# Performance work log

Measured on AMD Instinct MI355X. Metric: run time of the kernel, lower is better.

Reference implementation:

```python
import jax, jax.numpy as jnp
import numpy as np

DIM = 1024
HEADS = 16
B, N = 4, 1024

def setup_inputs() -> dict:
    key = jax.random.key(0)
    k1, k2, k3 = jax.random.split(key, 3)
    x = jax.random.normal(k1, (B, N, DIM), dtype=jnp.float32)
    # xavier-uniform-ish init scale
    Wqkv = jax.random.normal(k2, (3 * DIM, DIM), dtype=jnp.float32) * (1.0 / np.sqrt(DIM))
    bqkv = jnp.zeros((3 * DIM,), dtype=jnp.float32)
    W1 = jax.random.normal(k3, (DIM, DIM), dtype=jnp.float32) * (1.0 / np.sqrt(DIM))
    b1 = jnp.zeros((DIM,), dtype=jnp.float32)
    return {"x": x, "Wqkv": Wqkv, "bqkv": bqkv, "W1": W1, "b1": b1}

def reference(x, Wqkv, bqkv, W1, b1):
    b, n, dim = x.shape
    h = HEADS
    d = dim // h
    scale = dim ** (-0.5)  # NOTE: module scales by full dim, not head dim
    qkv = x @ Wqkv.T + bqkv  # [b, n, 3*dim]
    qkv = qkv.reshape(b, n, 3, h, d)
    q = jnp.transpose(qkv[:, :, 0], (0, 2, 1, 3))  # [b, h, n, d]
    k = jnp.transpose(qkv[:, :, 1], (0, 2, 1, 3))
    v = jnp.transpose(qkv[:, :, 2], (0, 2, 1, 3))
    dots = jnp.einsum('bhid,bhjd->bhij', q, k) * scale
    attn = jax.nn.softmax(dots, axis=-1)
    out = jnp.einsum('bhij,bhjd->bhid', attn, v)
    out = jnp.transpose(out, (0, 2, 1, 3)).reshape(b, n, dim)
    out = out @ W1.T + b1
    return out
```

## Files before the change

kernel.cpp:

```cpp
#include <hip/hip_runtime.h>
#include <cmath>

typedef __bf16 bf16;
typedef __bf16 bf16x8 __attribute__((ext_vector_type(8)));
typedef __bf16 bf16x4 __attribute__((ext_vector_type(4)));
typedef float f32x4 __attribute__((ext_vector_type(4)));

#define MFMA16(a, b, c) __builtin_amdgcn_mfma_f32_16x16x32_bf16(a, b, c, 0, 0, 0)

__device__ __forceinline__ void load_lds16(const void* g, void* l) {
    __builtin_amdgcn_global_load_lds(
        (const __attribute__((address_space(1))) void*)g,
        (__attribute__((address_space(3))) void*)l, 16, 0, 0);
}

__device__ __forceinline__ bf16x8 load8(const bf16* p) { return *(const bf16x8*)p; }
__device__ __forceinline__ bf16x8 load8(const float* p) {
    float4 f0 = *(const float4*)p;
    float4 f1 = *(const float4*)(p + 4);
    bf16x8 r;
    r[0] = (bf16)f0.x; r[1] = (bf16)f0.y; r[2] = (bf16)f0.z; r[3] = (bf16)f0.w;
    r[4] = (bf16)f1.x; r[5] = (bf16)f1.y; r[6] = (bf16)f1.z; r[7] = (bf16)f1.w;
    return r;
}

__global__ __launch_bounds__(256) void cvt3(
    const float* __restrict__ s0, bf16* __restrict__ d0, int n0,
    const float* __restrict__ s1, bf16* __restrict__ d1, int n1,
    const float* __restrict__ s2, bf16* __restrict__ d2, int n2)
{
    int i = blockIdx.x * 256 + threadIdx.x;
    const float* s; bf16* d; int base;
    if (i < n0)                { s = s0; d = d0; base = i; }
    else if (i < n0 + n1)      { s = s1; d = d1; base = i - n0; }
    else if (i < n0 + n1 + n2) { s = s2; d = d2; base = i - n0 - n1; }
    else return;
    *(bf16x8*)(d + (size_t)base * 8) = load8(s + (size_t)base * 8);
}

template <int EPI, typename TB, int BN>
__global__ __launch_bounds__(256) void gemm_bt(
    const bf16* __restrict__ A, const TB* __restrict__ Bm,
    const float* __restrict__ bias,
    bf16* __restrict__ qo, bf16* __restrict__ ko, bf16* __restrict__ vto,
    float* __restrict__ C, int M, int N, int K)
{
    constexpr int WN = BN / 2;
    constexpr int JN = WN / 16;
    constexpr int SLOTS = (128 + BN) * 8;

    __shared__ bf16 As[128 * 64];
    __shared__ bf16 Bs[BN * 64];

    const int tid = threadIdx.x;
    const int l   = tid & 63;
    const int w   = tid >> 6;
    const int wm  = w & 1, wn = w >> 1;
    const int l15 = l & 15;
    const int g   = l >> 4;
    const int swz = l15 & 7;
    const int m0  = blockIdx.y * 128;
    const int n0  = blockIdx.x * BN;

    f32x4 acc[4][JN] = {};

    for (int k0 = 0; k0 < K; k0 += 64) {
        __syncthreads();
        #pragma unroll
        for (int it = 0; it < SLOTS / 256; ++it) {
            int s = it * 256 + w * 64 + l;
            if (s < 1024) {
                int row = s >> 3, pc = s & 7;
                int lc  = pc ^ (row & 7);
                load_lds16(A + (size_t)(m0 + row) * K + k0 + lc * 8, &As[s * 8]);
            } else {
                int t = s - 1024;
                int row = t >> 3, pc = t & 7;
                int lc  = pc ^ (row & 7);
                if constexpr (sizeof(TB) == 2) {
                    load_lds16(Bm + (size_t)(n0 + row) * K + k0 + lc * 8, &Bs[t * 8]);
                } else {
                    *(bf16x8*)&Bs[t * 8] = load8(Bm + (size_t)(n0 + row) * K + k0 + lc * 8);
                }
            }
        }
        __syncthreads();
        #pragma unroll
        for (int kk = 0; kk < 64; kk += 32) {
            bf16x8 aF[4], bF[JN];
            #pragma unroll
            for (int i = 0; i < 4; ++i)
                aF[i] = *(const bf16x8*)&As[(wm * 64 + i * 16 + l15) * 64
                                            + ((((kk >> 3) + g) ^ swz) * 8)];
            #pragma unroll
            for (int j = 0; j < JN; ++j)
                bF[j] = *(const bf16x8*)&Bs[(wn * WN + j * 16 + l15) * 64
                                            + ((((kk >> 3) + g) ^ swz) * 8)];
            #pragma unroll
            for (int i = 0; i < 4; ++i)
                #pragma unroll
                for (int j = 0; j < JN; ++j)
                    acc[i][j] = MFMA16(aF[i], bF[j], acc[i][j]);
        }
    }

    #pragma unroll
    for (int j = 0; j < JN; ++j) {
        int gcol = n0 + wn * WN + j * 16 + l15;
        float bv = bias[gcol];
        if (EPI == 0) {
            int which = gcol >> 10;
            int h  = (gcol >> 6) & 15;
            int dd = gcol & 63;
            if (which == 2) {
                #pragma unroll
                for (int i = 0; i < 4; ++i) {
                    int grow0 = m0 + wm * 64 + i * 16 + g * 4;
                    int b     = grow0 >> 10;
                    int npos  = grow0 & 1023;
                    size_t bh = (size_t)(b * 16 + h);
                    bf16x4 pv;
                    #pragma unroll
                    for (int r = 0; r < 4; ++r)
                        pv[r] = (bf16)(acc[i][j][r] + bv);
                    *(bf16x4*)&vto[(bh * 64 + dd) * 1024 + npos] = pv;
                }
            } else {
                #pragma unroll
                for (int i = 0; i < 4; ++i) {
                    #pragma unroll
                    for (int r = 0; r < 4; ++r) {
                        int grow = m0 + wm * 64 + i * 16 + g * 4 + r;
                        int b    = grow >> 10;
                        int npos = grow & 1023;
                        float v  = acc[i][j][r] + bv;
                        size_t bh = (size_t)(b * 16 + h);
                        if (which == 0)
                            qo[(bh * 1024 + npos) * 64 + dd] = (bf16)v;
                        else
                            ko[(bh * 1024 + npos) * 64 + dd] = (bf16)v;
                    }
                }
            }
        } else {
            #pragma unroll
            for (int i = 0; i < 4; ++i)
                #pragma unroll
                for (int r = 0; r < 4; ++r) {
                    int grow = m0 + wm * 64 + i * 16 + g * 4 + r;
                    C[(size_t)grow * N + gcol] = acc[i][j][r] + bv;
                }
        }
    }
}

__global__ __launch_bounds__(256) void attn_fused(
    const bf16* __restrict__ qb, const bf16* __restrict__ kb,
    const bf16* __restrict__ vtb, bf16* __restrict__ attn)
{
    __shared__ bf16 Ks[2][64 * 64];
    __shared__ bf16 Vts[2][64 * 64];
    __shared__ bf16 Ps[4][16][40];

    const int tid = threadIdx.x;
    const int l   = tid & 63;
    const int w   = tid >> 6;
    const int l15 = l & 15;
    const int g   = l >> 4;
    const int swz = l15 & 7;
    const int bid = blockIdx.x;
    const int bh  = bid & 63;
    const int qc  = bid >> 6;
    const int m0  = qc * 64;

    const bf16* q_bh  = qb  + (size_t)bh * 65536;
    const bf16* k_bh  = kb  + (size_t)bh * 65536;
    const bf16* vt_bh = vtb + (size_t)bh * 65536;

    bf16x8 qf[2];
    #pragma unroll
    for (int kk = 0; kk < 2; ++kk)
        qf[kk] = *(const bf16x8*)(q_bh + (size_t)(m0 + w * 16 + l15) * 64
                                  + kk * 32 + g * 8);

    f32x4 o[4] = {};
    float lsum = 0.f;

    const float C_EXP = 0.04508422f;

    auto stage = [&](int buf, int j0) {
        #pragma unroll
        for (int it = 0; it < 2; ++it) {
            int s   = it * 256 + w * 64 + l;
            int row = s >> 3, pc = s & 7;
            int lc  = pc ^ (row & 7);
            load_lds16(k_bh + (size_t)(j0 + row) * 64 + lc * 8, &Ks[buf][s * 8]);
            load_lds16(vt_bh + (size_t)row * 1024 + j0 + lc * 8, &Vts[buf][s * 8]);
        }
    };

    stage(0, 0);

    for (int t = 0; t < 16; ++t) {
        const int c = t & 1;
        __syncthreads();
        if (t < 15) stage(c ^ 1, (t + 1) * 64);

        f32x4 s4[4] = {};
        #pragma unroll
        for (int kk = 0; kk < 2; ++kk) {
            bf16x8 kf[4];
            #pragma unroll
            for (int js = 0; js < 4; ++js)
                kf[js] = *(const bf16x8*)&Ks[c][(js * 16 + l15) * 64
                                                + (((kk * 4 + g) ^ swz) * 8)];
            __builtin_amdgcn_s_setprio(1);
            #pragma unroll
            for (int js = 0; js < 4; ++js)
                s4[js] = MFMA16(kf[js], qf[kk], s4[js]);
            __builtin_amdgcn_s_setprio(0);
        }

        #pragma unroll
        for (int h = 0; h < 2; ++h) {
            #pragma unroll
            for (int jsl = 0; jsl < 2; ++jsl) {
                int js = h * 2 + jsl;
                bf16x4 pk;
                float ps = 0.f;
                #pragma unroll
                for (int r = 0; r < 4; ++r) {
                    float p = exp2f(s4[js][r] * C_EXP);
                    ps += p;
                    pk[r] = (bf16)p;
                }
                lsum += ps;
                *(bf16x4*)&Ps[w][l15][jsl * 16 + g * 4] = pk;
            }
            bf16x8 vf[4];
            #pragma unroll
            for (int ns = 0; ns < 4; ++ns)
                vf[ns] = *(const bf16x8*)&Vts[c][(ns * 16 + l15) * 64
                                                 + (((h * 4 + g) ^ swz) * 8)];
            bf16x8 pf = *(const bf16x8*)&Ps[w][l15][g * 8];
            __builtin_amdgcn_s_setprio(1);
            #pragma unroll
            for (int ns = 0; ns < 4; ++ns)
                o[ns] = MFMA16(pf, vf[ns], o[ns]);
            __builtin_amdgcn_s_setprio(0);
        }
    }

    float t = lsum;
    t += __shfl_xor(t, 16);
    t += __shfl_xor(t, 32);

    #pragma unroll
    for (int r = 0; r < 4; ++r) {
        float inv = 1.0f / __shfl(t, g * 4 + r);
        int grow = m0 + w * 16 + g * 4 + r;
        size_t obase = ((size_t)(bh >> 4) * 1024 + grow) * 1024 + (bh & 15) * 64;
        #pragma unroll
        for (int ns = 0; ns < 4; ++ns)
            attn[obase + ns * 16 + l15] = (bf16)(o[ns][r] * inv);
    }
}

extern "C" void kernel_launch(void* const* d_in, const int* in_sizes, int n_in,
                              void* d_out, int out_size, void* d_ws, size_t ws_size,
                              hipStream_t stream)
{
    const float* x    = (const float*)d_in[0];
    const float* Wqkv = (const float*)d_in[1];
    const float* bqkv = (const float*)d_in[2];
    const float* W1   = (const float*)d_in[3];
    const float* b1   = (const float*)d_in[4];
    float* out = (float*)d_out;

    const size_t SEG = (size_t)4 * 16 * 1024 * 64;
    bf16* xbf  = (bf16*)d_ws;
    bf16* qb   = xbf + SEG;
    bf16* kb   = qb + SEG;
    bf16* vtb  = kb + SEG;
    bf16* attnb = xbf;
    bf16* wqkvbf = vtb + SEG;
    bf16* w1bf   = wqkvbf + 3145728;

    const bool cw = ws_size >= (size_t)(5 * SEG) * sizeof(bf16);

    const int nx = 524288;
    const int nw = cw ? 393216 : 0;
    const int n1 = cw ? 131072 : 0;
    const int tot = nx + nw + n1;
    cvt3<<<dim3((tot + 255) / 256), 256, 0, stream>>>(
        x, xbf, nx, Wqkv, wqkvbf, nw, W1, w1bf, n1);

    if (cw)
        gemm_bt<0, bf16, 128><<<dim3(24, 32), 256, 0, stream>>>(
            xbf, wqkvbf, bqkv, qb, kb, vtb, nullptr, 4096, 3072, 1024);
    else
        gemm_bt<0, float, 128><<<dim3(24, 32), 256, 0, stream>>>(
            xbf, Wqkv, bqkv, qb, kb, vtb, nullptr, 4096, 3072, 1024);

    attn_fused<<<dim3(1024), 256, 0, stream>>>(qb, kb, vtb, attnb);

    if (cw)
        gemm_bt<1, bf16, 64><<<dim3(16, 32), 256, 0, stream>>>(
            attnb, w1bf, b1, nullptr, nullptr, nullptr, out, 4096, 1024, 1024);
    else
        gemm_bt<1, float, 64><<<dim3(16, 32), 256, 0, stream>>>(
            attnb, W1, b1, nullptr, nullptr, nullptr, out, 4096, 1024, 1024);
}
```

Before: 166.1 us.

## Split attention KV tile across two warp halves with LDS reduction

The attention kernel now launches 512 threads per block. Each pair of waves shares the same 16 query rows but handles half of the key columns in each 64-key tile, so per-wave work per tile drops by half. The partial outputs and denominators are then summed through LDS at the end. The P staging buffer also gets an XOR swizzle in place of padding to avoid bank conflicts. This raises the number of active waves to hide latency, at the cost of a final cross-wave reduction and extra barriers.

```diff
diff --git a/kernel.cpp b/kernel.cpp
--- a/kernel.cpp
+++ b/kernel.cpp
@@ -154,17 +154,19 @@
     }
 }
 
-__global__ __launch_bounds__(256) void attn_fused(
+__global__ __launch_bounds__(512, 8) void attn_fused(
     const bf16* __restrict__ qb, const bf16* __restrict__ kb,
     const bf16* __restrict__ vtb, bf16* __restrict__ attn)
 {
     __shared__ bf16 Ks[2][64 * 64];
     __shared__ bf16 Vts[2][64 * 64];
-    __shared__ bf16 Ps[4][16][40];
+    __shared__ bf16 Ps[8][16][32];
 
     const int tid = threadIdx.x;
     const int l   = tid & 63;
     const int w   = tid >> 6;
+    const int wq  = w & 3;
+    const int wh  = w >> 2;
     const int l15 = l & 15;
     const int g   = l >> 4;
     const int swz = l15 & 7;
@@ -180,7 +182,7 @@
     bf16x8 qf[2];
     #pragma unroll
     for (int kk = 0; kk < 2; ++kk)
-        qf[kk] = *(const bf16x8*)(q_bh + (size_t)(m0 + w * 16 + l15) * 64
+        qf[kk] = *(const bf16x8*)(q_bh + (size_t)(m0 + wq * 16 + l15) * 64
                                   + kk * 32 + g * 8);
 
     f32x4 o[4] = {};
@@ -189,14 +191,11 @@
     const float C_EXP = 0.04508422f;
 
     auto stage = [&](int buf, int j0) {
-        #pragma unroll
-        for (int it = 0; it < 2; ++it) {
-            int s   = it * 256 + w * 64 + l;
-            int row = s >> 3, pc = s & 7;
-            int lc  = pc ^ (row & 7);
-            load_lds16(k_bh + (size_t)(j0 + row) * 64 + lc * 8, &Ks[buf][s * 8]);
-            load_lds16(vt_bh + (size_t)row * 1024 + j0 + lc * 8, &Vts[buf][s * 8]);
-        }
+        int s   = tid;
+        int row = s >> 3, pc = s & 7;
+        int lc  = pc ^ (row & 7);
+        load_lds16(k_bh + (size_t)(j0 + row) * 64 + lc * 8, &Ks[buf][s * 8]);
+        load_lds16(vt_bh + (size_t)row * 1024 + j0 + lc * 8, &Vts[buf][s * 8]);
     };
 
     stage(0, 0);
@@ -206,63 +205,78 @@
         __syncthreads();
         if (t < 15) stage(c ^ 1, (t + 1) * 64);
 
-        f32x4 s4[4] = {};
+        f32x4 s4[2] = {};
         #pragma unroll
         for (int kk = 0; kk < 2; ++kk) {
-            bf16x8 kf[4];
-            #pragma unroll
-            for (int js = 0; js < 4; ++js)
-                kf[js] = *(const bf16x8*)&Ks[c][(js * 16 + l15) * 64
-                                                + (((kk * 4 + g) ^ swz) * 8)];
+            bf16x8 kf[2];
+            #pragma unroll
+            for (int jsl = 0; jsl < 2; ++jsl)
+                kf[jsl] = *(const bf16x8*)&Ks[c][((wh * 2 + jsl) * 16 + l15) * 64
+                                                 + (((kk * 4 + g) ^ swz) * 8)];
             __builtin_amdgcn_s_setprio(1);
             #pragma unroll
-            for (int js = 0; js < 4; ++js)
-                s4[js] = MFMA16(kf[js], qf[kk], s4[js]);
+            for (int jsl = 0; jsl < 2; ++jsl)
+                s4[jsl] = MFMA16(kf[jsl], qf[kk], s4[jsl]);
             __builtin_amdgcn_s_setprio(0);
         }
 
         #pragma unroll
-        for (int h = 0; h < 2; ++h) {
-            #pragma unroll
-            for (int jsl = 0; jsl < 2; ++jsl) {
-                int js = h * 2 + jsl;
-                bf16x4 pk;
-                float ps = 0.f;
-                #pragma unroll
-                for (int r = 0; r < 4; ++r) {
-                    float p = exp2f(s4[js][r] * C_EXP);
-                    ps += p;
-                    pk[r] = (bf16)p;
-                }
-                lsum += ps;
-                *(bf16x4*)&Ps[w][l15][jsl * 16 + g * 4] = pk;
+        for (int jsl = 0; jsl < 2; ++jsl) {
+            bf16x4 pk;
+            float ps = 0.f;
+            #pragma unroll
+            for (int r = 0; r < 4; ++r) {
+                float p = exp2f(s4[jsl][r] * C_EXP);
+                ps += p;
+                pk[r] = (bf16)p;
             }
-            bf16x8 vf[4];
+            lsum += ps;
+            *(bf16x4*)&Ps[w][l15][(((jsl * 2 + (g >> 1)) ^ (l15 & 3)) * 8)
+                                  + (g & 1) * 4] = pk;
+        }
+
+        bf16x8 vf[4];
+        #pragma unroll
+        for (int ns = 0; ns < 4; ++ns)
+            vf[ns] = *(const bf16x8*)&Vts[c][(ns * 16 + l15) * 64
+                                             + (((wh * 4 + g) ^ swz) * 8)];
+        bf16x8 pf = *(const bf16x8*)&Ps[w][l15][(g ^ (l15 & 3)) * 8];
+        __builtin_amdgcn_s_setprio(1);
+        #pragma unroll
+        for (int ns = 0; ns < 4; ++ns)
+            o[ns] = MFMA16(pf, vf[ns], o[ns]);
+        __builtin_amdgcn_s_setprio(0);
+    }
+
+    float tden = lsum;
+    tden += __shfl_xor(tden, 16);
+    tden += __shfl_xor(tden, 32);
+
+    float* R  = (float*)&Ks[0][0];
+    float* DN = (float*)&Vts[0][0];
+    __syncthreads();
+    if (wh == 1) {
+        #pragma unroll
+        for (int ns = 0; ns < 4; ++ns)
+            *(f32x4*)&R[((wq * 64 + l) * 4 + ns) * 4] = o[ns];
+        DN[wq * 64 + l] = tden;
+    }
+    __syncthreads();
+    if (wh == 0) {
+        #pragma unroll
+        for (int ns = 0; ns < 4; ++ns)
+            o[ns] += *(const f32x4*)&R[((wq * 64 + l) * 4 + ns) * 4];
+        tden += DN[wq * 64 + l];
+
+        #pragma unroll
+        for (int r = 0; r < 4; ++r) {
+            float inv = 1.0f / __shfl(tden, g * 4 + r);
+            int grow = m0 + wq * 16 + g * 4 + r;
+            size_t obase = ((size_t)(bh >> 4) * 1024 + grow) * 1024 + (bh & 15) * 64;
             #pragma unroll
             for (int ns = 0; ns < 4; ++ns)
-                vf[ns] = *(const bf16x8*)&Vts[c][(ns * 16 + l15) * 64
-                                                 + (((h * 4 + g) ^ swz) * 8)];
-            bf16x8 pf = *(const bf16x8*)&Ps[w][l15][g * 8];
-            __builtin_amdgcn_s_setprio(1);
-            #pragma unroll
-            for (int ns = 0; ns < 4; ++ns)
-                o[ns] = MFMA16(pf, vf[ns], o[ns]);
-            __builtin_amdgcn_s_setprio(0);
-        }
-    }
-
-    float t = lsum;
-    t += __shfl_xor(t, 16);
-    t += __shfl_xor(t, 32);
-
-    #pragma unroll
-    for (int r = 0; r < 4; ++r) {
-        float inv = 1.0f / __shfl(t, g * 4 + r);
-        int grow = m0 + w * 16 + g * 4 + r;
-        size_t obase = ((size_t)(bh >> 4) * 1024 + grow) * 1024 + (bh & 15) * 64;
-        #pragma unroll
-        for (int ns = 0; ns < 4; ++ns)
-            attn[obase + ns * 16 + l15] = (bf16)(o[ns][r] * inv);
+                attn[obase + ns * 16 + l15] = (bf16)(o[ns][r] * inv);
+        }
     }
 }
 
@@ -302,7 +316,7 @@
         gemm_bt<0, float, 128><<<dim3(24, 32), 256, 0, stream>>>(
             xbf, Wqkv, bqkv, qb, kb, vtb, nullptr, 4096, 3072, 1024);
 
-    attn_fused<<<dim3(1024), 256, 0, stream>>>(qb, kb, vtb, attnb);
+    attn_fused<<<dim3(1024), 512, 0, stream>>>(qb, kb, vtb, attnb);
 
     if (cw)
         gemm_bt<1, bf16, 64><<<dim3(16, 32), 256, 0, stream>>>(
```

Result: no change. 164.9 us (-0.7%).
